# Kernel optimization log

Hardware: AMD Instinct MI355X
Metric: run time of the kernel (lower is better)

## Reference

```python
import jax, jax.numpy as jnp
import numpy as np

LENGTH = 4096
BATCH = 4096
N_OBS = 2


def setup_inputs() -> dict:
    key = jax.random.key(0)
    k1, k2, k3 = jax.random.split(key, 3)
    # Scale potentials down: the original chain performs no message
    # normalization, so we keep per-step log-growth tiny to avoid overflow.
    j = jax.random.normal(k1, (), dtype=jnp.float32) * 0.01
    b = jax.random.normal(k2, (N_OBS,), dtype=jnp.float32) * 0.01
    observations = jax.random.randint(k3, (BATCH, LENGTH), 0, N_OBS, dtype=jnp.int32)
    return {"j": j, "b": b, "observations": observations}


def reference(j, b, observations):
    # Max-product belief propagation on a binary-state chain CRF,
    # vectorized over the batch and scanned over the chain length.
    B, L = observations.shape
    values = jnp.array([-0.5, 0.5], dtype=jnp.float32)          # states {0,1} - 0.5
    pairs = values[:, None] * values[None, :]                    # [2,2] outer product
    psi = jnp.exp(j * pairs)                                     # [2,2] pairwise potential
    # Unary potentials phi[b_idx, i, s] = exp(b[obs] * values[s])
    phi = jnp.exp(b[observations][..., None] * values)           # [B,L,2]
    phi_tm = jnp.transpose(phi, (1, 0, 2))                       # time-major [L,B,2]

    def step(msg, phi_t):
        # msg_new[k] = max_l phi_t[l] * msg[l] * psi[k,l]
        x = phi_t * msg                                          # [B,2]
        new = jnp.max(x[:, None, :] * psi[None, :, :], axis=2)   # [B,2]
        return new, new

    ones = jnp.ones((B, 2), dtype=phi.dtype)
    # Forward messages: column 0 is ones, column t uses obs[0..t-1]
    _, fwd_msgs = jax.lax.scan(step, ones, phi_tm[:-1])          # [L-1,B,2]
    forward = jnp.concatenate([ones[None], fwd_msgs], axis=0)    # [L,B,2]
    # Backward messages: iterate i = L-1 .. 1, last column is ones
    _, bwd_msgs = jax.lax.scan(step, ones, phi_tm[1:][::-1])     # [L-1,B,2]
    backward = jnp.concatenate([bwd_msgs[::-1], ones[None]], axis=0)  # [L,B,2]

    beliefs = phi_tm * forward * backward                        # [L,B,2]
    return jnp.transpose(beliefs, (1, 2, 0))                     # [B,2,L]
```

## Files before the change

kernel.cpp:

```cpp
#include <hip/hip_runtime.h>
#include <math.h>

#define LENGTH 4096
#define BATCH  4096
#define CHUNK  8
#define NTHR   512
#define NWAVE  (NTHR / 64)

typedef float vf4 __attribute__((ext_vector_type(4)));

__device__ __forceinline__ void mp_compose(
    float a00, float a01, float a10, float a11,
    float b00, float b01, float b10, float b11,
    float& d00, float& d01, float& d10, float& d11) {
  d00 = fmaxf(a00 + b00, a01 + b10);
  d01 = fmaxf(a00 + b01, a01 + b11);
  d10 = fmaxf(a10 + b00, a11 + b10);
  d11 = fmaxf(a10 + b01, a11 + b11);
}

__device__ __forceinline__ void mp_step(
    float& f00, float& f01, float& f10, float& f11, float ui, float q) {
  float a0l0 = f00 - ui, a1l0 = f10 + ui;
  float a0l1 = f01 - ui, a1l1 = f11 + ui;
  float n00 = fmaxf(a0l0 + q, a1l0 - q);
  float n10 = fmaxf(a0l0 - q, a1l0 + q);
  float n01 = fmaxf(a0l1 + q, a1l1 - q);
  float n11 = fmaxf(a0l1 - q, a1l1 + q);
  f00 = n00; f01 = n01; f10 = n10; f11 = n11;
}

__global__ __launch_bounds__(NTHR, 8) void chain_bp_kernel(
    const float* __restrict__ jp, const float* __restrict__ bp,
    const int* __restrict__ obs, float* __restrict__ out) {
  const int row  = blockIdx.x;
  const int tid  = threadIdx.x;
  const int lane = tid & 63;
  const int wv   = tid >> 6;

  const float LOG2E = 1.44269504088896f;
  const float j  = jp[0];
  const float q  = 0.25f * j * LOG2E;
  const float u0 = 0.5f * bp[0] * LOG2E;
  const float u1 = 0.5f * bp[1] * LOG2E;
  const float wb = -fabsf(q);

  __shared__ vf4 lut4s[16];
  __shared__ vf4 lut8[256];
  __shared__ float smp[NWAVE][4];
  __shared__ float sms[NWAVE][4];

  const int t0 = tid * CHUNK;
  const int4* op = reinterpret_cast<const int4*>(obs + (size_t)row * LENGTH + t0);
  int4 o0 = op[0], o1 = op[1];
  float u[CHUNK];
  u[0]=o0.x?u1:u0; u[1]=o0.y?u1:u0; u[2]=o0.z?u1:u0; u[3]=o0.w?u1:u0;
  u[4]=o1.x?u1:u0; u[5]=o1.y?u1:u0; u[6]=o1.z?u1:u0; u[7]=o1.w?u1:u0;
  int idx = o0.x | (o0.y<<1) | (o0.z<<2) | (o0.w<<3)
          | (o1.x<<4) | (o1.y<<5) | (o1.z<<6) | (o1.w<<7);

  if (tid < 16) {
    float ua = (tid & 1) ? u1 : u0;
    float f00 = -ua + q, f01 = ua - q, f10 = -ua - q, f11 = ua + q;
#pragma unroll
    for (int k = 1; k < 4; ++k)
      mp_step(f00, f01, f10, f11, ((tid >> k) & 1) ? u1 : u0, q);
    lut4s[tid] = (vf4){f00, f01, f10, f11};
  }
  __syncthreads();
  if (tid < 256) {
    vf4 a = lut4s[tid >> 4], c = lut4s[tid & 15];
    float d00, d01, d10, d11;
    mp_compose(a[0], a[1], a[2], a[3], c[0], c[1], c[2], c[3], d00, d01, d10, d11);
    lut8[tid] = (vf4){d00, d01, d10, d11};
  }
  __syncthreads();

  vf4 Fm = lut8[idx];
  float f00 = Fm[0], f01 = Fm[1], f10 = Fm[2], f11 = Fm[3];

  float x00 = f00, x01 = f01, x10 = f10, x11 = f11;
  float y00 = f00, y01 = f10, y10 = f01, y11 = f11;
#pragma unroll
  for (int d = 1; d < 64; d <<= 1) {
    float px00 = __shfl_up(x00, d), px01 = __shfl_up(x01, d);
    float px10 = __shfl_up(x10, d), px11 = __shfl_up(x11, d);
    float py00 = __shfl_down(y00, d), py01 = __shfl_down(y01, d);
    float py10 = __shfl_down(y10, d), py11 = __shfl_down(y11, d);
    if (lane >= d) {
      float n00, n01, n10, n11;
      mp_compose(x00, x01, x10, x11, px00, px01, px10, px11, n00, n01, n10, n11);
      x00 = n00; x01 = n01; x10 = n10; x11 = n11;
    }
    if (lane + d < 64) {
      float n00, n01, n10, n11;
      mp_compose(y00, y01, y10, y11, py00, py01, py10, py11, n00, n01, n10, n11);
      y00 = n00; y01 = n01; y10 = n10; y11 = n11;
    }
  }

  if (lane == 63) { smp[wv][0] = x00; smp[wv][1] = x01; smp[wv][2] = x10; smp[wv][3] = x11; }
  if (lane == 0)  { sms[wv][0] = y00; sms[wv][1] = y01; sms[wv][2] = y10; sms[wv][3] = y11; }
  __syncthreads();

  float fh0 = 0.f, fh1 = 0.f;
  for (int k = 0; k < wv; ++k) {
    float m00 = smp[k][0], m01 = smp[k][1], m10 = smp[k][2], m11 = smp[k][3];
    float n0 = fmaxf(m00 + fh0, m01 + fh1);
    float n1 = fmaxf(m10 + fh0, m11 + fh1);
    fh0 = n0; fh1 = n1;
  }
  float wt0 = wb, wt1 = wb;
  for (int k = NWAVE - 1; k > wv; --k) {
    float m00 = sms[k][0], m01 = sms[k][1], m10 = sms[k][2], m11 = sms[k][3];
    float n0 = fmaxf(m00 + wt0, m01 + wt1);
    float n1 = fmaxf(m10 + wt0, m11 + wt1);
    wt0 = n0; wt1 = n1;
  }

  float z0 = fmaxf(x00 + fh0, x01 + fh1);
  float z1 = fmaxf(x10 + fh0, x11 + fh1);
  float zp0 = __shfl_up(z0, 1), zp1 = __shfl_up(z1, 1);
  float fi0 = (lane == 0) ? fh0 : zp0;
  float fi1 = (lane == 0) ? fh1 : zp1;

  float yv0 = fmaxf(y00 + wt0, y01 + wt1);
  float yv1 = fmaxf(y10 + wt0, y11 + wt1);
  float yn0 = __shfl_down(yv0, 1), yn1 = __shfl_down(yv1, 1);
  float wc0 = (lane == 63) ? wt0 : yn0;
  float wc1 = (lane == 63) ? wt1 : yn1;
  float g0 = fmaxf(q + wc0, -q + wc1);
  float g1 = fmaxf(-q + wc0, q + wc1);

  float b0[CHUNK], b1[CHUNK];
  b0[CHUNK - 1] = g0; b1[CHUNK - 1] = g1;
#pragma unroll
  for (int i = CHUNK - 1; i > 0; --i) {
    float ui = u[i];
    float a0 = b0[i] - ui;
    float a1 = b1[i] + ui;
    b0[i - 1] = fmaxf(a0 + q, a1 - q);
    b1[i - 1] = fmaxf(a0 - q, a1 + q);
  }

  float fw0 = fi0, fw1 = fi1;
  vf4 p0lo, p0hi, p1lo, p1hi;
#pragma unroll
  for (int i = 0; i < CHUNK; ++i) {
    float ui = u[i];
    float e0 = __builtin_amdgcn_exp2f(-ui + fw0 + b0[i]);
    float e1 = __builtin_amdgcn_exp2f( ui + fw1 + b1[i]);
    if (i < 4) { p0lo[i] = e0; p1lo[i] = e1; }
    else       { p0hi[i - 4] = e0; p1hi[i - 4] = e1; }
    float a0 = fw0 - ui, a1 = fw1 + ui;
    fw0 = fmaxf(a0 + q, a1 - q);
    fw1 = fmaxf(a0 - q, a1 + q);
  }
  float* outp = out + (size_t)row * (2 * LENGTH) + t0;
  *reinterpret_cast<vf4*>(outp)              = p0lo;
  *reinterpret_cast<vf4*>(outp + 4)          = p0hi;
  *reinterpret_cast<vf4*>(outp + LENGTH)     = p1lo;
  *reinterpret_cast<vf4*>(outp + LENGTH + 4) = p1hi;
}

extern "C" void kernel_launch(void* const* d_in, const int* in_sizes, int n_in,
                              void* d_out, int out_size, void* d_ws, size_t ws_size,
                              hipStream_t stream) {
  const float* jp  = (const float*)d_in[0];
  const float* bp  = (const float*)d_in[1];
  const int*   obs = (const int*)d_in[2];
  float* out = (float*)d_out;

  chain_bp_kernel<<<BATCH, NTHR, 0, stream>>>(jp, bp, obs, out);
}
```

Baseline: 189.3 us.

## Use 4-element chunks with 1024 threads and drop the shared LUT build

Each thread now handles 4 chain positions instead of 8, and the block grows to 1024 threads (16 waves). The per-chunk transfer matrix is computed directly with three max-plus steps, replacing the two-stage shared-memory lookup table and its two barriers. Output stores become nontemporal 16-byte writes. In exchange, the cross-wave serial combine gets longer, shuffle-scan work doubles, and the larger blocks with launch bounds of 8 may press on registers and occupancy.

```diff
diff --git a/kernel.cpp b/kernel.cpp
--- a/kernel.cpp
+++ b/kernel.cpp
@@ -3,8 +3,8 @@
 
 #define LENGTH 4096
 #define BATCH  4096
-#define CHUNK  8
-#define NTHR   512
+#define CHUNK  4
+#define NTHR   1024
 #define NWAVE  (NTHR / 64)
 
 typedef float vf4 __attribute__((ext_vector_type(4)));
@@ -45,39 +45,21 @@
   const float u1 = 0.5f * bp[1] * LOG2E;
   const float wb = -fabsf(q);
 
-  __shared__ vf4 lut4s[16];
-  __shared__ vf4 lut8[256];
   __shared__ float smp[NWAVE][4];
   __shared__ float sms[NWAVE][4];
 
   const int t0 = tid * CHUNK;
-  const int4* op = reinterpret_cast<const int4*>(obs + (size_t)row * LENGTH + t0);
-  int4 o0 = op[0], o1 = op[1];
+  int4 o0 = *reinterpret_cast<const int4*>(obs + (size_t)row * LENGTH + t0);
   float u[CHUNK];
-  u[0]=o0.x?u1:u0; u[1]=o0.y?u1:u0; u[2]=o0.z?u1:u0; u[3]=o0.w?u1:u0;
-  u[4]=o1.x?u1:u0; u[5]=o1.y?u1:u0; u[6]=o1.z?u1:u0; u[7]=o1.w?u1:u0;
-  int idx = o0.x | (o0.y<<1) | (o0.z<<2) | (o0.w<<3)
-          | (o1.x<<4) | (o1.y<<5) | (o1.z<<6) | (o1.w<<7);
+  u[0] = o0.x ? u1 : u0;
+  u[1] = o0.y ? u1 : u0;
+  u[2] = o0.z ? u1 : u0;
+  u[3] = o0.w ? u1 : u0;
 
-  if (tid < 16) {
-    float ua = (tid & 1) ? u1 : u0;
-    float f00 = -ua + q, f01 = ua - q, f10 = -ua - q, f11 = ua + q;
-#pragma unroll
-    for (int k = 1; k < 4; ++k)
-      mp_step(f00, f01, f10, f11, ((tid >> k) & 1) ? u1 : u0, q);
-    lut4s[tid] = (vf4){f00, f01, f10, f11};
-  }
-  __syncthreads();
-  if (tid < 256) {
-    vf4 a = lut4s[tid >> 4], c = lut4s[tid & 15];
-    float d00, d01, d10, d11;
-    mp_compose(a[0], a[1], a[2], a[3], c[0], c[1], c[2], c[3], d00, d01, d10, d11);
-    lut8[tid] = (vf4){d00, d01, d10, d11};
-  }
-  __syncthreads();
-
-  vf4 Fm = lut8[idx];
-  float f00 = Fm[0], f01 = Fm[1], f10 = Fm[2], f11 = Fm[3];
+  float f00 = -u[0] + q, f01 = u[0] - q, f10 = -u[0] - q, f11 = u[0] + q;
+  mp_step(f00, f01, f10, f11, u[1], q);
+  mp_step(f00, f01, f10, f11, u[2], q);
+  mp_step(f00, f01, f10, f11, u[3], q);
 
   float x00 = f00, x01 = f01, x10 = f10, x11 = f11;
   float y00 = f00, y01 = f10, y10 = f01, y11 = f11;
@@ -144,23 +126,19 @@
   }
 
   float fw0 = fi0, fw1 = fi1;
-  vf4 p0lo, p0hi, p1lo, p1hi;
+  vf4 p0, p1;
 #pragma unroll
   for (int i = 0; i < CHUNK; ++i) {
     float ui = u[i];
-    float e0 = __builtin_amdgcn_exp2f(-ui + fw0 + b0[i]);
-    float e1 = __builtin_amdgcn_exp2f( ui + fw1 + b1[i]);
-    if (i < 4) { p0lo[i] = e0; p1lo[i] = e1; }
-    else       { p0hi[i - 4] = e0; p1hi[i - 4] = e1; }
+    p0[i] = __builtin_amdgcn_exp2f(-ui + fw0 + b0[i]);
+    p1[i] = __builtin_amdgcn_exp2f( ui + fw1 + b1[i]);
     float a0 = fw0 - ui, a1 = fw1 + ui;
     fw0 = fmaxf(a0 + q, a1 - q);
     fw1 = fmaxf(a0 - q, a1 + q);
   }
   float* outp = out + (size_t)row * (2 * LENGTH) + t0;
-  *reinterpret_cast<vf4*>(outp)              = p0lo;
-  *reinterpret_cast<vf4*>(outp + 4)          = p0hi;
-  *reinterpret_cast<vf4*>(outp + LENGTH)     = p1lo;
-  *reinterpret_cast<vf4*>(outp + LENGTH + 4) = p1hi;
+  __builtin_nontemporal_store(p0, reinterpret_cast<vf4*>(outp));
+  __builtin_nontemporal_store(p1, reinterpret_cast<vf4*>(outp + LENGTH));
 }
 
 extern "C" void kernel_launch(void* const* d_in, const int* in_sizes, int n_in,
```

Result: slower. 195.5 us (+3.3%).

## Process four rows per block, amortizing LUT setup and prefetching next row

Applied to the files above, without the earlier changes.

Each block now handles four batch rows instead of one. The shared lookup tables are built once per block and reused across those rows. The next row's observations are loaded before the current row is processed, and double-buffered shared scratch avoids an extra barrier between rows. Output stores become nontemporal. The cost is fewer blocks in flight and more registers from the unrolled row loop.

```diff
diff --git a/kernel.cpp b/kernel.cpp
--- a/kernel.cpp
+++ b/kernel.cpp
@@ -6,6 +6,8 @@
 #define CHUNK  8
 #define NTHR   512
 #define NWAVE  (NTHR / 64)
+#define ROWS   4
+#define GRID   (BATCH / ROWS)
 
 typedef float vf4 __attribute__((ext_vector_type(4)));
 
@@ -33,7 +35,6 @@
 __global__ __launch_bounds__(NTHR, 8) void chain_bp_kernel(
     const float* __restrict__ jp, const float* __restrict__ bp,
     const int* __restrict__ obs, float* __restrict__ out) {
-  const int row  = blockIdx.x;
   const int tid  = threadIdx.x;
   const int lane = tid & 63;
   const int wv   = tid >> 6;
@@ -47,17 +48,14 @@
 
   __shared__ vf4 lut4s[16];
   __shared__ vf4 lut8[256];
-  __shared__ float smp[NWAVE][4];
-  __shared__ float sms[NWAVE][4];
+  __shared__ float smp[2][NWAVE][4];
+  __shared__ float sms[2][NWAVE][4];
 
-  const int t0 = tid * CHUNK;
-  const int4* op = reinterpret_cast<const int4*>(obs + (size_t)row * LENGTH + t0);
-  int4 o0 = op[0], o1 = op[1];
-  float u[CHUNK];
-  u[0]=o0.x?u1:u0; u[1]=o0.y?u1:u0; u[2]=o0.z?u1:u0; u[3]=o0.w?u1:u0;
-  u[4]=o1.x?u1:u0; u[5]=o1.y?u1:u0; u[6]=o1.z?u1:u0; u[7]=o1.w?u1:u0;
-  int idx = o0.x | (o0.y<<1) | (o0.z<<2) | (o0.w<<3)
-          | (o1.x<<4) | (o1.y<<5) | (o1.z<<6) | (o1.w<<7);
+  const int row0 = blockIdx.x * ROWS;
+  const int t0   = tid * CHUNK;
+
+  const int4* op0 = reinterpret_cast<const int4*>(obs + (size_t)row0 * LENGTH + t0);
+  int4 o0 = op0[0], o1 = op0[1];
 
   if (tid < 16) {
     float ua = (tid & 1) ? u1 : u0;
@@ -76,91 +74,109 @@
   }
   __syncthreads();
 
-  vf4 Fm = lut8[idx];
-  float f00 = Fm[0], f01 = Fm[1], f10 = Fm[2], f11 = Fm[3];
+#pragma unroll
+  for (int r = 0; r < ROWS; ++r) {
+    const int p = r & 1;
 
-  float x00 = f00, x01 = f01, x10 = f10, x11 = f11;
-  float y00 = f00, y01 = f10, y10 = f01, y11 = f11;
+    int4 c0 = o0, c1 = o1;
+    if (r + 1 < ROWS) {
+      const int4* np = reinterpret_cast<const int4*>(
+          obs + (size_t)(row0 + r + 1) * LENGTH + t0);
+      o0 = np[0]; o1 = np[1];
+    }
+
+    float u[CHUNK];
+    u[0]=c0.x?u1:u0; u[1]=c0.y?u1:u0; u[2]=c0.z?u1:u0; u[3]=c0.w?u1:u0;
+    u[4]=c1.x?u1:u0; u[5]=c1.y?u1:u0; u[6]=c1.z?u1:u0; u[7]=c1.w?u1:u0;
+    int idx = c0.x | (c0.y<<1) | (c0.z<<2) | (c0.w<<3)
+            | (c1.x<<4) | (c1.y<<5) | (c1.z<<6) | (c1.w<<7);
+
+    vf4 Fm = lut8[idx];
+    float f00 = Fm[0], f01 = Fm[1], f10 = Fm[2], f11 = Fm[3];
+
+    float x00 = f00, x01 = f01, x10 = f10, x11 = f11;
+    float y00 = f00, y01 = f10, y10 = f01, y11 = f11;
 #pragma unroll
-  for (int d = 1; d < 64; d <<= 1) {
-    float px00 = __shfl_up(x00, d), px01 = __shfl_up(x01, d);
-    float px10 = __shfl_up(x10, d), px11 = __shfl_up(x11, d);
-    float py00 = __shfl_down(y00, d), py01 = __shfl_down(y01, d);
-    float py10 = __shfl_down(y10, d), py11 = __shfl_down(y11, d);
-    if (lane >= d) {
-      float n00, n01, n10, n11;
-      mp_compose(x00, x01, x10, x11, px00, px01, px10, px11, n00, n01, n10, n11);
-      x00 = n00; x01 = n01; x10 = n10; x11 = n11;
+    for (int d = 1; d < 64; d <<= 1) {
+      float px00 = __shfl_up(x00, d), px01 = __shfl_up(x01, d);
+      float px10 = __shfl_up(x10, d), px11 = __shfl_up(x11, d);
+      float py00 = __shfl_down(y00, d), py01 = __shfl_down(y01, d);
+      float py10 = __shfl_down(y10, d), py11 = __shfl_down(y11, d);
+      if (lane >= d) {
+        float n00, n01, n10, n11;
+        mp_compose(x00, x01, x10, x11, px00, px01, px10, px11, n00, n01, n10, n11);
+        x00 = n00; x01 = n01; x10 = n10; x11 = n11;
+      }
+      if (lane + d < 64) {
+        float n00, n01, n10, n11;
+        mp_compose(y00, y01, y10, y11, py00, py01, py10, py11, n00, n01, n10, n11);
+        y00 = n00; y01 = n01; y10 = n10; y11 = n11;
+      }
     }
-    if (lane + d < 64) {
-      float n00, n01, n10, n11;
-      mp_compose(y00, y01, y10, y11, py00, py01, py10, py11, n00, n01, n10, n11);
-      y00 = n00; y01 = n01; y10 = n10; y11 = n11;
+
+    if (lane == 63) { smp[p][wv][0] = x00; smp[p][wv][1] = x01; smp[p][wv][2] = x10; smp[p][wv][3] = x11; }
+    if (lane == 0)  { sms[p][wv][0] = y00; sms[p][wv][1] = y01; sms[p][wv][2] = y10; sms[p][wv][3] = y11; }
+    __syncthreads();
+
+    float fh0 = 0.f, fh1 = 0.f;
+    for (int k = 0; k < wv; ++k) {
+      float m00 = smp[p][k][0], m01 = smp[p][k][1], m10 = smp[p][k][2], m11 = smp[p][k][3];
+      float n0 = fmaxf(m00 + fh0, m01 + fh1);
+      float n1 = fmaxf(m10 + fh0, m11 + fh1);
+      fh0 = n0; fh1 = n1;
     }
+    float wt0 = wb, wt1 = wb;
+    for (int k = NWAVE - 1; k > wv; --k) {
+      float m00 = sms[p][k][0], m01 = sms[p][k][1], m10 = sms[p][k][2], m11 = sms[p][k][3];
+      float n0 = fmaxf(m00 + wt0, m01 + wt1);
+      float n1 = fmaxf(m10 + wt0, m11 + wt1);
+      wt0 = n0; wt1 = n1;
+    }
+
+    float z0 = fmaxf(x00 + fh0, x01 + fh1);
+    float z1 = fmaxf(x10 + fh0, x11 + fh1);
+    float zp0 = __shfl_up(z0, 1), zp1 = __shfl_up(z1, 1);
+    float fi0 = (lane == 0) ? fh0 : zp0;
+    float fi1 = (lane == 0) ? fh1 : zp1;
+
+    float yv0 = fmaxf(y00 + wt0, y01 + wt1);
+    float yv1 = fmaxf(y10 + wt0, y11 + wt1);
+    float yn0 = __shfl_down(yv0, 1), yn1 = __shfl_down(yv1, 1);
+    float wc0 = (lane == 63) ? wt0 : yn0;
+    float wc1 = (lane == 63) ? wt1 : yn1;
+    float g0 = fmaxf(q + wc0, -q + wc1);
+    float g1 = fmaxf(-q + wc0, q + wc1);
+
+    float b0[CHUNK], b1[CHUNK];
+    b0[CHUNK - 1] = g0; b1[CHUNK - 1] = g1;
+#pragma unroll
+    for (int i = CHUNK - 1; i > 0; --i) {
+      float ui = u[i];
+      float a0 = b0[i] - ui;
+      float a1 = b1[i] + ui;
+      b0[i - 1] = fmaxf(a0 + q, a1 - q);
+      b1[i - 1] = fmaxf(a0 - q, a1 + q);
+    }
+
+    float fw0 = fi0, fw1 = fi1;
+    vf4 p0lo, p0hi, p1lo, p1hi;
+#pragma unroll
+    for (int i = 0; i < CHUNK; ++i) {
+      float ui = u[i];
+      float e0 = __builtin_amdgcn_exp2f(-ui + fw0 + b0[i]);
+      float e1 = __builtin_amdgcn_exp2f( ui + fw1 + b1[i]);
+      if (i < 4) { p0lo[i] = e0; p1lo[i] = e1; }
+      else       { p0hi[i - 4] = e0; p1hi[i - 4] = e1; }
+      float a0 = fw0 - ui, a1 = fw1 + ui;
+      fw0 = fmaxf(a0 + q, a1 - q);
+      fw1 = fmaxf(a0 - q, a1 + q);
+    }
+    float* outp = out + (size_t)(row0 + r) * (2 * LENGTH) + t0;
+    __builtin_nontemporal_store(p0lo, reinterpret_cast<vf4*>(outp));
+    __builtin_nontemporal_store(p0hi, reinterpret_cast<vf4*>(outp + 4));
+    __builtin_nontemporal_store(p1lo, reinterpret_cast<vf4*>(outp + LENGTH));
+    __builtin_nontemporal_store(p1hi, reinterpret_cast<vf4*>(outp + LENGTH + 4));
   }
-
-  if (lane == 63) { smp[wv][0] = x00; smp[wv][1] = x01; smp[wv][2] = x10; smp[wv][3] = x11; }
-  if (lane == 0)  { sms[wv][0] = y00; sms[wv][1] = y01; sms[wv][2] = y10; sms[wv][3] = y11; }
-  __syncthreads();
-
-  float fh0 = 0.f, fh1 = 0.f;
-  for (int k = 0; k < wv; ++k) {
-    float m00 = smp[k][0], m01 = smp[k][1], m10 = smp[k][2], m11 = smp[k][3];
-    float n0 = fmaxf(m00 + fh0, m01 + fh1);
-    float n1 = fmaxf(m10 + fh0, m11 + fh1);
-    fh0 = n0; fh1 = n1;
-  }
-  float wt0 = wb, wt1 = wb;
-  for (int k = NWAVE - 1; k > wv; --k) {
-    float m00 = sms[k][0], m01 = sms[k][1], m10 = sms[k][2], m11 = sms[k][3];
-    float n0 = fmaxf(m00 + wt0, m01 + wt1);
-    float n1 = fmaxf(m10 + wt0, m11 + wt1);
-    wt0 = n0; wt1 = n1;
-  }
-
-  float z0 = fmaxf(x00 + fh0, x01 + fh1);
-  float z1 = fmaxf(x10 + fh0, x11 + fh1);
-  float zp0 = __shfl_up(z0, 1), zp1 = __shfl_up(z1, 1);
-  float fi0 = (lane == 0) ? fh0 : zp0;
-  float fi1 = (lane == 0) ? fh1 : zp1;
-
-  float yv0 = fmaxf(y00 + wt0, y01 + wt1);
-  float yv1 = fmaxf(y10 + wt0, y11 + wt1);
-  float yn0 = __shfl_down(yv0, 1), yn1 = __shfl_down(yv1, 1);
-  float wc0 = (lane == 63) ? wt0 : yn0;
-  float wc1 = (lane == 63) ? wt1 : yn1;
-  float g0 = fmaxf(q + wc0, -q + wc1);
-  float g1 = fmaxf(-q + wc0, q + wc1);
-
-  float b0[CHUNK], b1[CHUNK];
-  b0[CHUNK - 1] = g0; b1[CHUNK - 1] = g1;
-#pragma unroll
-  for (int i = CHUNK - 1; i > 0; --i) {
-    float ui = u[i];
-    float a0 = b0[i] - ui;
-    float a1 = b1[i] + ui;
-    b0[i - 1] = fmaxf(a0 + q, a1 - q);
-    b1[i - 1] = fmaxf(a0 - q, a1 + q);
-  }
-
-  float fw0 = fi0, fw1 = fi1;
-  vf4 p0lo, p0hi, p1lo, p1hi;
-#pragma unroll
-  for (int i = 0; i < CHUNK; ++i) {
-    float ui = u[i];
-    float e0 = __builtin_amdgcn_exp2f(-ui + fw0 + b0[i]);
-    float e1 = __builtin_amdgcn_exp2f( ui + fw1 + b1[i]);
-    if (i < 4) { p0lo[i] = e0; p1lo[i] = e1; }
-    else       { p0hi[i - 4] = e0; p1hi[i - 4] = e1; }
-    float a0 = fw0 - ui, a1 = fw1 + ui;
-    fw0 = fmaxf(a0 + q, a1 - q);
-    fw1 = fmaxf(a0 - q, a1 + q);
-  }
-  float* outp = out + (size_t)row * (2 * LENGTH) + t0;
-  *reinterpret_cast<vf4*>(outp)              = p0lo;
-  *reinterpret_cast<vf4*>(outp + 4)          = p0hi;
-  *reinterpret_cast<vf4*>(outp + LENGTH)     = p1lo;
-  *reinterpret_cast<vf4*>(outp + LENGTH + 4) = p1hi;
 }
 
 extern "C" void kernel_launch(void* const* d_in, const int* in_sizes, int n_in,
@@ -171,5 +187,5 @@
   const int*   obs = (const int*)d_in[2];
   float* out = (float*)d_out;
 
-  chain_bp_kernel<<<BATCH, NTHR, 0, stream>>>(jp, bp, obs, out);
+  chain_bp_kernel<<<GRID, NTHR, 0, stream>>>(jp, bp, obs, out);
 }
```

Measured after the change: 214.4 us. 13.3% more time.
